# Performance work log

Hardware: AMD Instinct MI355X
Metric: run time of the kernel (lower is better)

Reference implementation:

```python
import jax, jax.numpy as jnp
import numpy as np

HIDDEN = 16  # hk.LSTM(16)


def lstm_scan(x, W, b, reverse):
    """Haiku LSTM unroll. x: [B,T,D]; W: [D+H, 4H]; b: [4H]. Returns [B,T,H]."""
    B = x.shape[0]

    def step(carry, xt):
        h, c = carry
        gated = jnp.concatenate([xt, h], axis=-1) @ W + b
        i, g, f, o = jnp.split(gated, 4, axis=-1)
        f = jax.nn.sigmoid(f + 1.0)  # haiku forget-gate bias of +1
        c = f * c + jax.nn.sigmoid(i) * jnp.tanh(g)
        h = jax.nn.sigmoid(o) * jnp.tanh(c)
        return (h, c), h

    init = (jnp.zeros((B, HIDDEN), x.dtype), jnp.zeros((B, HIDDEN), x.dtype))
    xt = jnp.swapaxes(x, 0, 1)  # [T,B,D] time-major for scan
    _, outs = jax.lax.scan(step, init, xt, reverse=reverse)
    return jnp.swapaxes(outs, 0, 1)  # [B,T,H]


def setup_inputs() -> dict:
    key = jax.random.key(0)
    ks = jax.random.split(key, 8)
    B, T, D = 4096, 256, 20
    E, H, M, OUT = 64, HIDDEN, 16, 2

    def glorot(k, shape):
        fan_in = shape[0]
        return (jax.random.normal(k, shape, jnp.float32) / np.sqrt(fan_in)).astype(jnp.float32)

    return {
        "x": jax.random.normal(ks[0], (B, T, D), jnp.float32),
        "W0": glorot(ks[1], (D, E)), "b0": jnp.zeros((E,), jnp.float32),
        "Wf": glorot(ks[2], (E + H, 4 * H)), "bf": jnp.zeros((4 * H,), jnp.float32),
        "Wb": glorot(ks[3], (E + H, 4 * H)), "bb": jnp.zeros((4 * H,), jnp.float32),
        "W1": glorot(ks[4], (2 * H, E)), "b1": jnp.zeros((E,), jnp.float32),
        "W2": glorot(ks[5], (E, M)), "b2": jnp.zeros((M,), jnp.float32),
        "W3": glorot(ks[6], (M, OUT)), "b3": jnp.zeros((OUT,), jnp.float32),
    }


def reference(x, W0, b0, Wf, bf, Wb, bb, W1, b1, W2, b2, W3, b3):
    h = jax.nn.relu(x @ W0 + b0)                 # [B,T,64]
    fwd = lstm_scan(h, Wf, bf, reverse=False)    # [B,T,16]
    bwd = lstm_scan(h, Wb, bb, reverse=True)     # [B,T,16], output[t] uses future state
    outs = jnp.concatenate([fwd, bwd], axis=-1)[:, -1, :]  # take last time step, [B,32]
    outs = jax.nn.relu(outs @ W1 + b1)
    outs = jax.nn.relu(outs @ W2 + b2)
    return outs @ W3 + b3
```

## Files before the change

### kernel.cpp

```cpp
#include <hip/hip_runtime.h>


typedef __attribute__((ext_vector_type(8))) short short8;
typedef __attribute__((ext_vector_type(4))) float floatx4;

union F8 { uint32_t u[4]; short8 v; };
union H2 { uint32_t u; _Float16 h[2]; };

#define LDW  66
#define LDW2 68

#define LOG2E 1.44269504088896340736f

__device__ __forceinline__ float tanh_fast(float x) {
    float e = __expf(-2.f * x);
    return __fdividef(2.f, 1.f + e) - 1.f;
}

#define ROT(v, S) __int_as_float(__builtin_amdgcn_mov_dpp(__float_as_int(v), 0x120 | (S), 0xf, 0xf, false))

__device__ __forceinline__ void split_pack(const float* f, uint32_t* hi, uint32_t* lo) {
#pragma unroll
    for (int i = 0; i < 4; ++i) {
        uint32_t u0 = __float_as_uint(f[2 * i]), u1 = __float_as_uint(f[2 * i + 1]);
        hi[i] = __builtin_amdgcn_perm(u1, u0, 0x07060302u);
        float r0 = f[2 * i]     - __uint_as_float(u0 & 0xFFFF0000u);
        float r1 = f[2 * i + 1] - __uint_as_float(u1 & 0xFFFF0000u);
        lo[i] = __builtin_amdgcn_perm(__float_as_uint(r1), __float_as_uint(r0), 0x07060302u);
    }
}

__global__ __launch_bounds__(256, 2)
void gpre_gemm(const float* __restrict__ x,
               const float* __restrict__ W0, const float* __restrict__ b0,
               const float* __restrict__ Wf, const float* __restrict__ bf,
               uint32_t* __restrict__ gph)
{
    __shared__ __align__(16) float tA[4][16 * LDW2];
    __shared__ __align__(16) float tB[4][16 * LDW2];

    const int tid  = threadIdx.x;
    const int wv   = tid >> 6;
    const int j    = tid & 63;
    const int nl   = j & 15;
    const int quad = j >> 4;

    F8 B1h[4], B1l[4];
#pragma unroll
    for (int T = 0; T < 4; ++T) {
        float w[8];
#pragma unroll
        for (int e = 0; e < 8; ++e) {
            int k = quad * 8 + e;
            w[e] = (k < 20) ? W0[k * 64 + T * 16 + nl] : 0.f;
        }
        split_pack(w, B1h[T].u, B1l[T].u);
    }
    F8 B2h[4][2], B2l[4][2];
#pragma unroll
    for (int T = 0; T < 4; ++T)
#pragma unroll
        for (int KH = 0; KH < 2; ++KH) {
            float w[8];
#pragma unroll
            for (int e = 0; e < 8; ++e) {
                int k = KH * 32 + quad * 8 + e;
                w[e] = Wf[k * 64 + T * 16 + nl];
            }
            split_pack(w, B2h[T][KH].u, B2l[T][KH].u);
        }

    float b0v[4], bfv[4];
#pragma unroll
    for (int T = 0; T < 4; ++T) {
        b0v[T] = b0[T * 16 + nl];
        bfv[T] = bf[T * 16 + nl] + ((T == 2) ? 1.f : 0.f);
    }

    const size_t base = (size_t)(blockIdx.x * 4 + wv) * 256;

    float4 xp0, xp1;
    {
        const float* xr = x + (base + nl) * 20;
        if (quad < 2) {
            xp0 = *(const float4*)(xr + quad * 8);
            xp1 = *(const float4*)(xr + quad * 8 + 4);
        } else if (quad == 2) {
            xp0 = *(const float4*)(xr + 16);
            xp1 = (float4){0.f, 0.f, 0.f, 0.f};
        } else {
            xp0 = (float4){0.f, 0.f, 0.f, 0.f};
            xp1 = (float4){0.f, 0.f, 0.f, 0.f};
        }
    }

#pragma unroll 1
    for (int tile = 0; tile < 16; ++tile) {
        float xk[8] = {xp0.x, xp0.y, xp0.z, xp0.w, xp1.x, xp1.y, xp1.z, xp1.w};

        {
            int tn = (tile < 15) ? (tile + 1) : 15;
            const float* xr = x + (base + tn * 16 + nl) * 20;
            if (quad < 2) {
                xp0 = *(const float4*)(xr + quad * 8);
                xp1 = *(const float4*)(xr + quad * 8 + 4);
            } else if (quad == 2) {
                xp0 = *(const float4*)(xr + 16);
            }
        }

        F8 A1h, A1l;
        split_pack(xk, A1h.u, A1l.u);

        floatx4 acc1[4];
#pragma unroll
        for (int T = 0; T < 4; ++T) acc1[T] = (floatx4){b0v[T], b0v[T], b0v[T], b0v[T]};
#pragma unroll
        for (int T = 0; T < 4; ++T) {
            acc1[T] = __builtin_amdgcn_mfma_f32_16x16x32_bf16(A1h.v, B1h[T].v, acc1[T], 0, 0, 0);
            acc1[T] = __builtin_amdgcn_mfma_f32_16x16x32_bf16(A1l.v, B1h[T].v, acc1[T], 0, 0, 0);
            acc1[T] = __builtin_amdgcn_mfma_f32_16x16x32_bf16(A1h.v, B1l[T].v, acc1[T], 0, 0, 0);
        }

#pragma unroll
        for (int T = 0; T < 4; ++T)
#pragma unroll
            for (int reg = 0; reg < 4; ++reg)
                tA[wv][(quad * 4 + reg) * LDW2 + T * 16 + nl] = fmaxf(acc1[T][reg], 0.f);
        __builtin_amdgcn_wave_barrier();

        F8 A2h[2], A2l[2];
#pragma unroll
        for (int KH = 0; KH < 2; ++KH) {
            float xe[8];
#pragma unroll
            for (int e = 0; e < 8; ++e)
                xe[e] = tA[wv][nl * LDW2 + KH * 32 + quad * 8 + e];
            split_pack(xe, A2h[KH].u, A2l[KH].u);
        }

        floatx4 acc2[4];
#pragma unroll
        for (int T = 0; T < 4; ++T) acc2[T] = (floatx4){bfv[T], bfv[T], bfv[T], bfv[T]};
#pragma unroll
        for (int T = 0; T < 4; ++T)
#pragma unroll
            for (int KH = 0; KH < 2; ++KH) {
                acc2[T] = __builtin_amdgcn_mfma_f32_16x16x32_bf16(A2h[KH].v, B2h[T][KH].v, acc2[T], 0, 0, 0);
                acc2[T] = __builtin_amdgcn_mfma_f32_16x16x32_bf16(A2l[KH].v, B2h[T][KH].v, acc2[T], 0, 0, 0);
                acc2[T] = __builtin_amdgcn_mfma_f32_16x16x32_bf16(A2h[KH].v, B2l[T][KH].v, acc2[T], 0, 0, 0);
            }

#pragma unroll
        for (int T = 0; T < 4; ++T)
#pragma unroll
            for (int reg = 0; reg < 4; ++reg)
                tB[wv][(quad * 4 + reg) * LDW2 + T * 16 + nl] = acc2[T][reg];
        __builtin_amdgcn_wave_barrier();

        uint32_t* gp = gph + ((base >> 1) + tile * 8) * 64;
#pragma unroll
        for (int tp = 0; tp < 8; ++tp) {
            float a0 = tB[wv][(2 * tp) * LDW2 + j];
            float a1 = tB[wv][(2 * tp + 1) * LDW2 + j];
            H2 pk;
            pk.h[0] = (_Float16)a0;
            pk.h[1] = (_Float16)a1;
            gp[tp * 64 + j] = pk.u;
        }
        __builtin_amdgcn_wave_barrier();
    }
}

__global__ __launch_bounds__(256, 4)
void lstm_scan(const uint32_t* __restrict__ gph,
               const float* __restrict__ x,
               const float* __restrict__ W0, const float* __restrict__ b0,
               const float* __restrict__ Wf,
               const float* __restrict__ Wb, const float* __restrict__ bb,
               const float* __restrict__ W1, const float* __restrict__ b1,
               const float* __restrict__ W2, const float* __restrict__ b2,
               const float* __restrict__ W3, const float* __restrict__ b3,
               float* __restrict__ out)
{
    __shared__ __align__(16) float xh_sh[4][64];
    __shared__ __align__(16) float h_sh[4][48];

    const int wv   = threadIdx.x >> 6;
    const int j    = threadIdx.x & 63;
    const int b    = blockIdx.x * 4 + wv;
    const int nl   = j & 15;
    const int quad = j >> 4;

    int rot1 = __builtin_amdgcn_mov_dpp(j, 0x121, 0xf, 0xf, false);
    const bool plus = ((rot1 & 15) == ((nl + 1) & 15));

    float wfhp[16];
#pragma unroll
    for (int s = 0; s < 16; ++s) {
        const int srcq = plus ? ((nl + s) & 15) : ((nl + 16 - s) & 15);
        wfhp[s] = Wf[(64 + srcq) * 64 + j];
    }

    const float gmul  = (quad == 1) ? -2.f : -1.f;
    const float gmul2 = gmul * LOG2E;
    const float amul  = (quad == 1) ? 2.f : 1.f;
    const float aadd  = (quad == 1) ? -1.f : 0.f;

    const int adr_i = 4 * nl;
    const int adr_g = 4 * nl + 64;
    const int adr_f = 4 * nl + 128;
    const int adr_o = 4 * nl + 192;

    float c = 0.f, hh = 0.f;
    const uint32_t* gb = gph + (size_t)b * (128 * 64);

#define STEPG(G)                                                               \
    {                                                                          \
        float v0 = (G), v1, v2, v3;                                            \
        asm volatile(                                                          \
            "v_fmac_f32 %0, %4, %5\n\t"                                        \
            "s_nop 1\n\t"                                                      \
            "v_mul_f32_dpp %1, %4, %6 row_ror:1 row_mask:0xf bank_mask:0xf\n\t"  \
            "v_mul_f32_dpp %2, %4, %7 row_ror:2 row_mask:0xf bank_mask:0xf\n\t"  \
            "v_mul_f32_dpp %3, %4, %8 row_ror:3 row_mask:0xf bank_mask:0xf\n\t"  \
            "v_fmac_f32_dpp %0, %4, %9 row_ror:4 row_mask:0xf bank_mask:0xf\n\t" \
            "v_fmac_f32_dpp %1, %4, %10 row_ror:5 row_mask:0xf bank_mask:0xf\n\t" \
            "v_fmac_f32_dpp %2, %4, %11 row_ror:6 row_mask:0xf bank_mask:0xf\n\t" \
            "v_fmac_f32_dpp %3, %4, %12 row_ror:7 row_mask:0xf bank_mask:0xf\n\t" \
            "v_fmac_f32_dpp %0, %4, %13 row_ror:8 row_mask:0xf bank_mask:0xf\n\t" \
            "v_fmac_f32_dpp %1, %4, %14 row_ror:9 row_mask:0xf bank_mask:0xf\n\t" \
            "v_fmac_f32_dpp %2, %4, %15 row_ror:10 row_mask:0xf bank_mask:0xf\n\t" \
            "v_fmac_f32_dpp %3, %4, %16 row_ror:11 row_mask:0xf bank_mask:0xf\n\t" \
            "v_fmac_f32_dpp %0, %4, %17 row_ror:12 row_mask:0xf bank_mask:0xf\n\t" \
            "v_fmac_f32_dpp %1, %4, %18 row_ror:13 row_mask:0xf bank_mask:0xf\n\t" \
            "v_fmac_f32_dpp %2, %4, %19 row_ror:14 row_mask:0xf bank_mask:0xf\n\t" \
            "v_fmac_f32_dpp %3, %4, %20 row_ror:15 row_mask:0xf bank_mask:0xf"   \
            : "+&v"(v0), "=&v"(v1), "=&v"(v2), "=&v"(v3)                       \
            : "v"(hh),                                                         \
              "v"(wfhp[0]),  "v"(wfhp[1]),  "v"(wfhp[2]),  "v"(wfhp[3]),       \
              "v"(wfhp[4]),  "v"(wfhp[5]),  "v"(wfhp[6]),  "v"(wfhp[7]),       \
              "v"(wfhp[8]),  "v"(wfhp[9]),  "v"(wfhp[10]), "v"(wfhp[11]),      \
              "v"(wfhp[12]), "v"(wfhp[13]), "v"(wfhp[14]), "v"(wfhp[15]));     \
        float gated = (v0 + v1) + (v2 + v3);                                   \
        float e = __builtin_amdgcn_exp2f(gmul2 * gated);                       \
        float y = __builtin_amdgcn_rcpf(1.f + e);                              \
        float a = fmaf(y, amul, aadd);                                         \
        int ab = __float_as_int(a);                                            \
        float ai = __int_as_float(__builtin_amdgcn_ds_bpermute(adr_i, ab));    \
        float ag = __int_as_float(__builtin_amdgcn_ds_bpermute(adr_g, ab));    \
        float af = __int_as_float(__builtin_amdgcn_ds_bpermute(adr_f, ab));    \
        float ao = __int_as_float(__builtin_amdgcn_ds_bpermute(adr_o, ab));    \
        c = fmaf(af, c, ai * ag);                                              \
        float e2 = __builtin_amdgcn_exp2f(-2.f * LOG2E * c);                   \
        float th = fmaf(__builtin_amdgcn_rcpf(1.f + e2), 2.f, -1.f);           \
        hh = ao * th;                                                          \
    }

    uint32_t bufA[8], bufB[8];
#pragma unroll
    for (int i = 0; i < 8; ++i) bufA[i] = gb[i * 64 + j];
#pragma unroll
    for (int i = 0; i < 8; ++i) bufB[i] = gb[(8 + i) * 64 + j];

#pragma unroll 1
    for (int blk = 0; blk < 16; blk += 2) {
#pragma unroll
        for (int p = 0; p < 8; ++p) {
            H2 u; u.u = bufA[p];
            float g0 = (float)u.h[0];
            float g1 = (float)u.h[1];
            STEPG(g0)
            STEPG(g1)
        }
        {
            int nb = blk + 2; nb = (nb > 15) ? 15 : nb;
#pragma unroll
            for (int i = 0; i < 8; ++i) bufA[i] = gb[(nb * 8 + i) * 64 + j];
        }
#pragma unroll
        for (int p = 0; p < 8; ++p) {
            H2 u; u.u = bufB[p];
            float g0 = (float)u.h[0];
            float g1 = (float)u.h[1];
            STEPG(g0)
            STEPG(g1)
        }
        {
            int nb = blk + 3; nb = (nb > 15) ? 15 : nb;
#pragma unroll
            for (int i = 0; i < 8; ++i) bufB[i] = gb[(nb * 8 + i) * 64 + j];
        }
    }
#undef STEPG

    {
        const float* xr = x + (size_t)b * (256 * 20) + 255 * 20;
        float s = b0[j];
#pragma unroll
        for (int k = 0; k < 20; ++k) s = fmaf(xr[k], W0[k * 64 + j], s);
        xh_sh[wv][j] = fmaxf(s, 0.f);
        if (j < 16) h_sh[wv][j] = hh;
    }
    __builtin_amdgcn_wave_barrier();

    {
        float u0 = bb[j], u1 = 0.f, u2 = 0.f, u3 = 0.f;
        const float* xr = xh_sh[wv];
#pragma unroll
        for (int k4 = 0; k4 < 16; ++k4) {
            u0 = fmaf(xr[4 * k4 + 0], Wb[(4 * k4 + 0) * 64 + j], u0);
            u1 = fmaf(xr[4 * k4 + 1], Wb[(4 * k4 + 1) * 64 + j], u1);
            u2 = fmaf(xr[4 * k4 + 2], Wb[(4 * k4 + 2) * 64 + j], u2);
            u3 = fmaf(xr[4 * k4 + 3], Wb[(4 * k4 + 3) * 64 + j], u3);
        }
        float gated = (u0 + u1) + (u2 + u3);
        float e = __expf(gmul * gated);
        float y = __fdividef(1.f, 1.f + e);
        float a = fmaf(y, amul, aadd);
        float ai = __shfl(a, nl, 64);
        float ag = __shfl(a, nl + 16, 64);
        float ao = __shfl(a, nl + 48, 64);
        float cb = ai * ag;
        float hb = ao * tanh_fast(cb);
        __builtin_amdgcn_wave_barrier();
        if (j < 16) h_sh[wv][16 + j] = hb;
        __builtin_amdgcn_wave_barrier();
    }

    {
        float u0 = b1[j], u1 = 0.f, u2 = 0.f, u3 = 0.f;
        const float4* hs = (const float4*)h_sh[wv];
#pragma unroll
        for (int k4 = 0; k4 < 8; ++k4) {
            float4 v = hs[k4];
            u0 = fmaf(v.x, W1[(4 * k4 + 0) * 64 + j], u0);
            u1 = fmaf(v.y, W1[(4 * k4 + 1) * 64 + j], u1);
            u2 = fmaf(v.z, W1[(4 * k4 + 2) * 64 + j], u2);
            u3 = fmaf(v.w, W1[(4 * k4 + 3) * 64 + j], u3);
        }
        float l1 = fmaxf((u0 + u1) + (u2 + u3), 0.f);
        __builtin_amdgcn_wave_barrier();
        xh_sh[wv][j] = l1;
        __builtin_amdgcn_wave_barrier();

        if (j < 16) {
            float v0 = b2[j], v1 = 0.f, v2 = 0.f, v3 = 0.f;
            const float4* ls = (const float4*)xh_sh[wv];
#pragma unroll
            for (int k4 = 0; k4 < 16; ++k4) {
                float4 v = ls[k4];
                v0 = fmaf(v.x, W2[(4 * k4 + 0) * 16 + j], v0);
                v1 = fmaf(v.y, W2[(4 * k4 + 1) * 16 + j], v1);
                v2 = fmaf(v.z, W2[(4 * k4 + 2) * 16 + j], v2);
                v3 = fmaf(v.w, W2[(4 * k4 + 3) * 16 + j], v3);
            }
            h_sh[wv][32 + j] = fmaxf((v0 + v1) + (v2 + v3), 0.f);
        }
        __builtin_amdgcn_wave_barrier();

        if (j < 2) {
            float o = b3[j];
#pragma unroll
            for (int k = 0; k < 16; ++k)
                o = fmaf(h_sh[wv][32 + k], W3[k * 2 + j], o);
            out[b * 2 + j] = o;
        }
    }
}

__global__ __launch_bounds__(64, 2)
void bilstm_fused_r4(const float* __restrict__ x,
                     const float* __restrict__ W0, const float* __restrict__ b0,
                     const float* __restrict__ Wf, const float* __restrict__ bf,
                     const float* __restrict__ Wb, const float* __restrict__ bb,
                     const float* __restrict__ W1, const float* __restrict__ b1,
                     const float* __restrict__ W2, const float* __restrict__ b2,
                     const float* __restrict__ W3, const float* __restrict__ b3,
                     float* __restrict__ out)
{
    __shared__ __align__(16) float lds_xh[16 * LDW];
    __shared__ __align__(16) float lds_g [16 * LDW];
    __shared__ __align__(16) float h_sh[48];

    const int j    = threadIdx.x;
    const int b    = blockIdx.x;
    const int nl   = j & 15;
    const int quad = j >> 4;

    int rot1 = __builtin_amdgcn_mov_dpp(j, 0x121, 0xf, 0xf, false);
    const bool plus = ((rot1 & 15) == ((nl + 1) & 15));

    float wfhp[16];
#pragma unroll
    for (int s = 0; s < 16; ++s) {
        const int srcq = plus ? ((nl + s) & 15) : ((nl + 16 - s) & 15);
        wfhp[s] = Wf[(64 + srcq) * 64 + j];
    }

    F8 B1h[4], B1l[4];
#pragma unroll
    for (int T = 0; T < 4; ++T) {
        float w[8];
#pragma unroll
        for (int e = 0; e < 8; ++e) {
            int k = quad * 8 + e;
            w[e] = (k < 20) ? W0[k * 64 + T * 16 + nl] : 0.f;
        }
        split_pack(w, B1h[T].u, B1l[T].u);
    }
    F8 B2h[4][2], B2l[4][2];
#pragma unroll
    for (int T = 0; T < 4; ++T)
#pragma unroll
        for (int KH = 0; KH < 2; ++KH) {
            float w[8];
#pragma unroll
            for (int e = 0; e < 8; ++e) {
                int k = KH * 32 + quad * 8 + e;
                w[e] = Wf[k * 64 + T * 16 + nl];
            }
            split_pack(w, B2h[T][KH].u, B2l[T][KH].u);
        }

    float b0v[4], bfv[4];
#pragma unroll
    for (int T = 0; T < 4; ++T) {
        b0v[T] = b0[T * 16 + nl];
        bfv[T] = bf[T * 16 + nl];
    }

    const float gmul  = (quad == 1) ? -2.f : -1.f;
    const float gbias = (quad == 2) ? 1.f : 0.f;
    const float amul  = (quad == 1) ? 2.f : 1.f;
    const float aadd  = (quad == 1) ? -1.f : 0.f;
    const bool  b0sel = (quad & 1) != 0;
    const bool  b1sel = (quad & 2) != 0;

    float c = 0.f, hh = 0.f;
    const float* xb = x + (size_t)b * (256 * 20);

#pragma unroll 1
    for (int ch = 0; ch < 16; ++ch) {
        const int t0 = ch * 16;
        const float* xrow = xb + (size_t)(t0 + nl) * 20;
        float xk[8];
#pragma unroll
        for (int e = 0; e < 8; ++e) {
            int k = quad * 8 + e;
            xk[e] = (k < 20) ? xrow[k] : 0.f;
        }
        F8 A1h, A1l;
        split_pack(xk, A1h.u, A1l.u);

        floatx4 acc1[4];
#pragma unroll
        for (int T = 0; T < 4; ++T) acc1[T] = (floatx4){b0v[T], b0v[T], b0v[T], b0v[T]};
#pragma unroll
        for (int T = 0; T < 4; ++T) {
            acc1[T] = __builtin_amdgcn_mfma_f32_16x16x32_bf16(A1h.v, B1h[T].v, acc1[T], 0, 0, 0);
            acc1[T] = __builtin_amdgcn_mfma_f32_16x16x32_bf16(A1l.v, B1h[T].v, acc1[T], 0, 0, 0);
            acc1[T] = __builtin_amdgcn_mfma_f32_16x16x32_bf16(A1h.v, B1l[T].v, acc1[T], 0, 0, 0);
        }
#pragma unroll
        for (int T = 0; T < 4; ++T)
#pragma unroll
            for (int reg = 0; reg < 4; ++reg)
                lds_xh[(quad * 4 + reg) * LDW + T * 16 + nl] = fmaxf(acc1[T][reg], 0.f);
        __builtin_amdgcn_wave_barrier();

        F8 A2h[2], A2l[2];
#pragma unroll
        for (int KH = 0; KH < 2; ++KH) {
            float xe[8];
#pragma unroll
            for (int e = 0; e < 8; ++e)
                xe[e] = lds_xh[nl * LDW + KH * 32 + quad * 8 + e];
            split_pack(xe, A2h[KH].u, A2l[KH].u);
        }

        floatx4 acc2[4];
#pragma unroll
        for (int T = 0; T < 4; ++T) acc2[T] = (floatx4){bfv[T], bfv[T], bfv[T], bfv[T]};
#pragma unroll
        for (int T = 0; T < 4; ++T)
#pragma unroll
            for (int KH = 0; KH < 2; ++KH) {
                acc2[T] = __builtin_amdgcn_mfma_f32_16x16x32_bf16(A2h[KH].v, B2h[T][KH].v, acc2[T], 0, 0, 0);
                acc2[T] = __builtin_amdgcn_mfma_f32_16x16x32_bf16(A2l[KH].v, B2h[T][KH].v, acc2[T], 0, 0, 0);
                acc2[T] = __builtin_amdgcn_mfma_f32_16x16x32_bf16(A2h[KH].v, B2l[T][KH].v, acc2[T], 0, 0, 0);
            }
#pragma unroll
        for (int T = 0; T < 4; ++T)
#pragma unroll
            for (int reg = 0; reg < 4; ++reg)
                lds_g[(quad * 4 + reg) * LDW + T * 16 + nl] = acc2[T][reg];
        __builtin_amdgcn_wave_barrier();

        float gcur = lds_g[j];
#pragma unroll
        for (int tau = 0; tau < 16; ++tau) {
            float gnext = lds_g[((tau < 15) ? (tau + 1) : 15) * LDW + j];
            float v0 = hh * wfhp[0];
            float v1 = ROT(hh, 1) * wfhp[1];
            float v2 = ROT(hh, 2) * wfhp[2];
            float v3 = ROT(hh, 3) * wfhp[3];
            v0 = fmaf(ROT(hh, 4),  wfhp[4],  v0);
            v1 = fmaf(ROT(hh, 5),  wfhp[5],  v1);
            v2 = fmaf(ROT(hh, 6),  wfhp[6],  v2);
            v3 = fmaf(ROT(hh, 7),  wfhp[7],  v3);
            v0 = fmaf(ROT(hh, 8),  wfhp[8],  v0);
            v1 = fmaf(ROT(hh, 9),  wfhp[9],  v1);
            v2 = fmaf(ROT(hh, 10), wfhp[10], v2);
            v3 = fmaf(ROT(hh, 11), wfhp[11], v3);
            v0 = fmaf(ROT(hh, 12), wfhp[12], v0);
            v1 = fmaf(ROT(hh, 13), wfhp[13], v1);
            v2 = fmaf(ROT(hh, 14), wfhp[14], v2);
            v3 = fmaf(ROT(hh, 15), wfhp[15], v3);
            float gated = gcur + ((v0 + v1) + (v2 + v3));

            float e = __expf(gmul * (gated + gbias));
            float y = __fdividef(1.f, 1.f + e);
            float a = fmaf(y, amul, aadd);

            float d1 = __shfl_xor(a, 16);
            float d2 = __shfl_xor(a, 32);
            float d3 = __shfl_xor(a, 48);
            float lo  = b0sel ? d1 : a;
            float hi  = b0sel ? d3 : d2;
            float lo1 = b0sel ? a  : d1;
            float hi1 = b0sel ? d2 : d3;
            float ai = b1sel ? hi  : lo;
            float ag = b1sel ? hi1 : lo1;
            float af = b1sel ? lo  : hi;
            float ao = b1sel ? lo1 : hi1;

            c  = fmaf(af, c, ai * ag);
            hh = ao * tanh_fast(c);
            gcur = gnext;
        }
    }

    if (j < 16) h_sh[j] = hh;
    __builtin_amdgcn_wave_barrier();

    {
        float u0 = bb[j], u1 = 0.f, u2 = 0.f, u3 = 0.f;
        const float* xr = &lds_xh[15 * LDW];
#pragma unroll
        for (int k4 = 0; k4 < 16; ++k4) {
            u0 = fmaf(xr[4 * k4 + 0], Wb[(4 * k4 + 0) * 64 + j], u0);
            u1 = fmaf(xr[4 * k4 + 1], Wb[(4 * k4 + 1) * 64 + j], u1);
            u2 = fmaf(xr[4 * k4 + 2], Wb[(4 * k4 + 2) * 64 + j], u2);
            u3 = fmaf(xr[4 * k4 + 3], Wb[(4 * k4 + 3) * 64 + j], u3);
        }
        float gated = (u0 + u1) + (u2 + u3);
        float e = __expf(gmul * gated);
        float y = __fdividef(1.f, 1.f + e);
        float a = fmaf(y, amul, aadd);
        float ai = __shfl(a, nl, 64);
        float ag = __shfl(a, nl + 16, 64);
        float ao = __shfl(a, nl + 48, 64);
        float cb = ai * ag;
        float hb = ao * tanh_fast(cb);
        __builtin_amdgcn_wave_barrier();
        if (j < 16) h_sh[16 + j] = hb;
        __builtin_amdgcn_wave_barrier();
    }

    {
        float u0 = b1[j], u1 = 0.f, u2 = 0.f, u3 = 0.f;
        const float4* hs = (const float4*)h_sh;
#pragma unroll
        for (int k4 = 0; k4 < 8; ++k4) {
            float4 v = hs[k4];
            u0 = fmaf(v.x, W1[(4 * k4 + 0) * 64 + j], u0);
            u1 = fmaf(v.y, W1[(4 * k4 + 1) * 64 + j], u1);
            u2 = fmaf(v.z, W1[(4 * k4 + 2) * 64 + j], u2);
            u3 = fmaf(v.w, W1[(4 * k4 + 3) * 64 + j], u3);
        }
        float l1 = fmaxf((u0 + u1) + (u2 + u3), 0.f);
        __builtin_amdgcn_wave_barrier();
        lds_g[j] = l1;
        __builtin_amdgcn_wave_barrier();

        if (j < 16) {
            float v0 = b2[j], v1 = 0.f, v2 = 0.f, v3 = 0.f;
            const float4* ls = (const float4*)lds_g;
#pragma unroll
            for (int k4 = 0; k4 < 16; ++k4) {
                float4 v = ls[k4];
                v0 = fmaf(v.x, W2[(4 * k4 + 0) * 16 + j], v0);
                v1 = fmaf(v.y, W2[(4 * k4 + 1) * 16 + j], v1);
                v2 = fmaf(v.z, W2[(4 * k4 + 2) * 16 + j], v2);
                v3 = fmaf(v.w, W2[(4 * k4 + 3) * 16 + j], v3);
            }
            h_sh[32 + j] = fmaxf((v0 + v1) + (v2 + v3), 0.f);
        }
        __builtin_amdgcn_wave_barrier();

        if (j < 2) {
            float o = b3[j];
#pragma unroll
            for (int k = 0; k < 16; ++k)
                o = fmaf(h_sh[32 + k], W3[k * 2 + j], o);
            out[b * 2 + j] = o;
        }
    }
}

extern "C" void kernel_launch(void* const* d_in, const int* in_sizes, int n_in,
                              void* d_out, int out_size, void* d_ws, size_t ws_size,
                              hipStream_t stream) {
    const float* x  = (const float*)d_in[0];
    const float* W0 = (const float*)d_in[1];
    const float* b0 = (const float*)d_in[2];
    const float* Wf = (const float*)d_in[3];
    const float* bf = (const float*)d_in[4];
    const float* Wb = (const float*)d_in[5];
    const float* bb = (const float*)d_in[6];
    const float* W1 = (const float*)d_in[7];
    const float* b1 = (const float*)d_in[8];
    const float* W2 = (const float*)d_in[9];
    const float* b2 = (const float*)d_in[10];
    const float* W3 = (const float*)d_in[11];
    const float* b3 = (const float*)d_in[12];
    float* outp = (float*)d_out;

    const size_t need = (size_t)4096 * 128 * 64 * sizeof(uint32_t);
    if (ws_size >= need) {
        uint32_t* gph = (uint32_t*)d_ws;
        hipLaunchKernelGGL(gpre_gemm, dim3(1024), dim3(256), 0, stream,
                           x, W0, b0, Wf, bf, gph);
        hipLaunchKernelGGL(lstm_scan, dim3(1024), dim3(256), 0, stream,
                           gph, x, W0, b0, Wf, Wb, bb, W1, b1, W2, b2, W3, b3, outp);
    } else {
        hipLaunchKernelGGL(bilstm_fused_r4, dim3(4096), dim3(64), 0, stream,
                           x, W0, b0, Wf, bf, Wb, bb, W1, b1, W2, b2, W3, b3, outp);
    }
}
```

Baseline: 261.9 us.

## Fold activation scales into LSTM weights and vectorize gate-precompute layout

The sigmoid/tanh exponent scale factors (-log2e, -2log2e) are folded into the precomputed input-projection weights, biases and recurrent weights, so each step drops a multiply. The cell state is kept in a pre-scaled domain by adjusting the g-gate affine, so tanh(c) needs no scale multiply either. The recurrent dot product now uses two accumulators instead of four, which removes adds but lengthens the dependency chain. The fp16 gate buffer layout becomes per-lane contiguous so writes and prefetches use 128-bit vector loads and stores instead of eight scalar accesses.

New measurement: 255.6 us, median of 4. 1.02x faster.

```diff
diff --git a/kernel.cpp b/kernel.cpp
--- a/kernel.cpp
+++ b/kernel.cpp
@@ -6,6 +6,7 @@
 
 union F8 { uint32_t u[4]; short8 v; };
 union H2 { uint32_t u; _Float16 h[2]; };
+union B8 { uint4 q[2]; uint32_t d[8]; };
 
 #define LDW  66
 #define LDW2 68
@@ -58,23 +59,26 @@
     }
     F8 B2h[4][2], B2l[4][2];
 #pragma unroll
-    for (int T = 0; T < 4; ++T)
+    for (int T = 0; T < 4; ++T) {
+        const float sgT = (T == 1) ? (-2.f * LOG2E) : (-LOG2E);
 #pragma unroll
         for (int KH = 0; KH < 2; ++KH) {
             float w[8];
 #pragma unroll
             for (int e = 0; e < 8; ++e) {
                 int k = KH * 32 + quad * 8 + e;
-                w[e] = Wf[k * 64 + T * 16 + nl];
+                w[e] = Wf[k * 64 + T * 16 + nl] * sgT;
             }
             split_pack(w, B2h[T][KH].u, B2l[T][KH].u);
         }
+    }
 
     float b0v[4], bfv[4];
 #pragma unroll
     for (int T = 0; T < 4; ++T) {
+        const float sgT = (T == 1) ? (-2.f * LOG2E) : (-LOG2E);
         b0v[T] = b0[T * 16 + nl];
-        bfv[T] = bf[T * 16 + nl] + ((T == 2) ? 1.f : 0.f);
+        bfv[T] = (bf[T * 16 + nl] + ((T == 2) ? 1.f : 0.f)) * sgT;
     }
 
     const size_t base = (size_t)(blockIdx.x * 4 + wv) * 256;
@@ -158,15 +162,20 @@
                 tB[wv][(quad * 4 + reg) * LDW2 + T * 16 + nl] = acc2[T][reg];
         __builtin_amdgcn_wave_barrier();
 
-        uint32_t* gp = gph + ((base >> 1) + tile * 8) * 64;
-#pragma unroll
-        for (int tp = 0; tp < 8; ++tp) {
-            float a0 = tB[wv][(2 * tp) * LDW2 + j];
-            float a1 = tB[wv][(2 * tp + 1) * LDW2 + j];
-            H2 pk;
-            pk.h[0] = (_Float16)a0;
-            pk.h[1] = (_Float16)a1;
-            gp[tp * 64 + j] = pk.u;
+        {
+            B8 r;
+#pragma unroll
+            for (int tp = 0; tp < 8; ++tp) {
+                float a0 = tB[wv][(2 * tp) * LDW2 + j];
+                float a1 = tB[wv][(2 * tp + 1) * LDW2 + j];
+                H2 pk;
+                pk.h[0] = (_Float16)a0;
+                pk.h[1] = (_Float16)a1;
+                r.d[tp] = pk.u;
+            }
+            uint32_t* gp = gph + ((size_t)(blockIdx.x * 4 + wv) * 16 + tile) * 512 + j * 8;
+            *(uint4*)(gp)     = r.q[0];
+            *(uint4*)(gp + 4) = r.q[1];
         }
         __builtin_amdgcn_wave_barrier();
     }
@@ -195,55 +204,57 @@
     int rot1 = __builtin_amdgcn_mov_dpp(j, 0x121, 0xf, 0xf, false);
     const bool plus = ((rot1 & 15) == ((nl + 1) & 15));
 
+    const float sj = (quad == 1) ? (-2.f * LOG2E) : (-LOG2E);
     float wfhp[16];
 #pragma unroll
     for (int s = 0; s < 16; ++s) {
         const int srcq = plus ? ((nl + s) & 15) : ((nl + 16 - s) & 15);
-        wfhp[s] = Wf[(64 + srcq) * 64 + j];
-    }
-
-    const float gmul  = (quad == 1) ? -2.f : -1.f;
-    const float gmul2 = gmul * LOG2E;
-    const float amul  = (quad == 1) ? 2.f : 1.f;
-    const float aadd  = (quad == 1) ? -1.f : 0.f;
+        wfhp[s] = Wf[(64 + srcq) * 64 + j] * sj;
+    }
+
+    const float amul = (quad == 1) ? (-4.f * LOG2E) : 1.f;
+    const float aadd = (quad == 1) ? ( 2.f * LOG2E) : 0.f;
+
+    const float gmulE = (quad == 1) ? -2.f : -1.f;
+    const float amulE = (quad == 1) ? 2.f : 1.f;
+    const float aaddE = (quad == 1) ? -1.f : 0.f;
 
     const int adr_i = 4 * nl;
     const int adr_g = 4 * nl + 64;
     const int adr_f = 4 * nl + 128;
     const int adr_o = 4 * nl + 192;
 
-    float c = 0.f, hh = 0.f;
-    const uint32_t* gb = gph + (size_t)b * (128 * 64);
+    float C = 0.f, hh = 0.f;
+    const uint32_t* gb = gph + (size_t)b * 8192;
 
 #define STEPG(G)                                                               \
     {                                                                          \
-        float v0 = (G), v1, v2, v3;                                            \
+        float v0 = (G), v1;                                                    \
         asm volatile(                                                          \
-            "v_fmac_f32 %0, %4, %5\n\t"                                        \
+            "v_fmac_f32 %0, %2, %3\n\t"                                        \
             "s_nop 1\n\t"                                                      \
-            "v_mul_f32_dpp %1, %4, %6 row_ror:1 row_mask:0xf bank_mask:0xf\n\t"  \
-            "v_mul_f32_dpp %2, %4, %7 row_ror:2 row_mask:0xf bank_mask:0xf\n\t"  \
-            "v_mul_f32_dpp %3, %4, %8 row_ror:3 row_mask:0xf bank_mask:0xf\n\t"  \
-            "v_fmac_f32_dpp %0, %4, %9 row_ror:4 row_mask:0xf bank_mask:0xf\n\t" \
-            "v_fmac_f32_dpp %1, %4, %10 row_ror:5 row_mask:0xf bank_mask:0xf\n\t" \
-            "v_fmac_f32_dpp %2, %4, %11 row_ror:6 row_mask:0xf bank_mask:0xf\n\t" \
-            "v_fmac_f32_dpp %3, %4, %12 row_ror:7 row_mask:0xf bank_mask:0xf\n\t" \
-            "v_fmac_f32_dpp %0, %4, %13 row_ror:8 row_mask:0xf bank_mask:0xf\n\t" \
-            "v_fmac_f32_dpp %1, %4, %14 row_ror:9 row_mask:0xf bank_mask:0xf\n\t" \
-            "v_fmac_f32_dpp %2, %4, %15 row_ror:10 row_mask:0xf bank_mask:0xf\n\t" \
-            "v_fmac_f32_dpp %3, %4, %16 row_ror:11 row_mask:0xf bank_mask:0xf\n\t" \
-            "v_fmac_f32_dpp %0, %4, %17 row_ror:12 row_mask:0xf bank_mask:0xf\n\t" \
-            "v_fmac_f32_dpp %1, %4, %18 row_ror:13 row_mask:0xf bank_mask:0xf\n\t" \
-            "v_fmac_f32_dpp %2, %4, %19 row_ror:14 row_mask:0xf bank_mask:0xf\n\t" \
-            "v_fmac_f32_dpp %3, %4, %20 row_ror:15 row_mask:0xf bank_mask:0xf"   \
-            : "+&v"(v0), "=&v"(v1), "=&v"(v2), "=&v"(v3)                       \
+            "v_mul_f32_dpp %1, %2, %4 row_ror:1 row_mask:0xf bank_mask:0xf\n\t"  \
+            "v_fmac_f32_dpp %0, %2, %5 row_ror:2 row_mask:0xf bank_mask:0xf\n\t" \
+            "v_fmac_f32_dpp %1, %2, %6 row_ror:3 row_mask:0xf bank_mask:0xf\n\t" \
+            "v_fmac_f32_dpp %0, %2, %7 row_ror:4 row_mask:0xf bank_mask:0xf\n\t" \
+            "v_fmac_f32_dpp %1, %2, %8 row_ror:5 row_mask:0xf bank_mask:0xf\n\t" \
+            "v_fmac_f32_dpp %0, %2, %9 row_ror:6 row_mask:0xf bank_mask:0xf\n\t" \
+            "v_fmac_f32_dpp %1, %2, %10 row_ror:7 row_mask:0xf bank_mask:0xf\n\t" \
+            "v_fmac_f32_dpp %0, %2, %11 row_ror:8 row_mask:0xf bank_mask:0xf\n\t" \
+            "v_fmac_f32_dpp %1, %2, %12 row_ror:9 row_mask:0xf bank_mask:0xf\n\t" \
+            "v_fmac_f32_dpp %0, %2, %13 row_ror:10 row_mask:0xf bank_mask:0xf\n\t" \
+            "v_fmac_f32_dpp %1, %2, %14 row_ror:11 row_mask:0xf bank_mask:0xf\n\t" \
+            "v_fmac_f32_dpp %0, %2, %15 row_ror:12 row_mask:0xf bank_mask:0xf\n\t" \
+            "v_fmac_f32_dpp %1, %2, %16 row_ror:13 row_mask:0xf bank_mask:0xf\n\t" \
+            "v_fmac_f32_dpp %0, %2, %17 row_ror:14 row_mask:0xf bank_mask:0xf\n\t" \
+            "v_fmac_f32_dpp %1, %2, %18 row_ror:15 row_mask:0xf bank_mask:0xf"   \
+            : "+&v"(v0), "=&v"(v1)                                             \
             : "v"(hh),                                                         \
               "v"(wfhp[0]),  "v"(wfhp[1]),  "v"(wfhp[2]),  "v"(wfhp[3]),       \
               "v"(wfhp[4]),  "v"(wfhp[5]),  "v"(wfhp[6]),  "v"(wfhp[7]),       \
               "v"(wfhp[8]),  "v"(wfhp[9]),  "v"(wfhp[10]), "v"(wfhp[11]),      \
               "v"(wfhp[12]), "v"(wfhp[13]), "v"(wfhp[14]), "v"(wfhp[15]));     \
-        float gated = (v0 + v1) + (v2 + v3);                                   \
-        float e = __builtin_amdgcn_exp2f(gmul2 * gated);                       \
+        float e = __builtin_amdgcn_exp2f(v0 + v1);                             \
         float y = __builtin_amdgcn_rcpf(1.f + e);                              \
         float a = fmaf(y, amul, aadd);                                         \
         int ab = __float_as_int(a);                                            \
@@ -251,23 +262,23 @@
         float ag = __int_as_float(__builtin_amdgcn_ds_bpermute(adr_g, ab));    \
         float af = __int_as_float(__builtin_amdgcn_ds_bpermute(adr_f, ab));    \
         float ao = __int_as_float(__builtin_amdgcn_ds_bpermute(adr_o, ab));    \
-        c = fmaf(af, c, ai * ag);                                              \
-        float e2 = __builtin_amdgcn_exp2f(-2.f * LOG2E * c);                   \
+        C = fmaf(af, C, ai * ag);                                              \
+        float e2 = __builtin_amdgcn_exp2f(C);                                  \
         float th = fmaf(__builtin_amdgcn_rcpf(1.f + e2), 2.f, -1.f);           \
         hh = ao * th;                                                          \
     }
 
-    uint32_t bufA[8], bufB[8];
-#pragma unroll
-    for (int i = 0; i < 8; ++i) bufA[i] = gb[i * 64 + j];
-#pragma unroll
-    for (int i = 0; i < 8; ++i) bufB[i] = gb[(8 + i) * 64 + j];
+    B8 bufA, bufB;
+    bufA.q[0] = *(const uint4*)(gb + j * 8);
+    bufA.q[1] = *(const uint4*)(gb + j * 8 + 4);
+    bufB.q[0] = *(const uint4*)(gb + 512 + j * 8);
+    bufB.q[1] = *(const uint4*)(gb + 512 + j * 8 + 4);
 
 #pragma unroll 1
     for (int blk = 0; blk < 16; blk += 2) {
 #pragma unroll
         for (int p = 0; p < 8; ++p) {
-            H2 u; u.u = bufA[p];
+            H2 u; u.u = bufA.d[p];
             float g0 = (float)u.h[0];
             float g1 = (float)u.h[1];
             STEPG(g0)
@@ -275,12 +286,12 @@
         }
         {
             int nb = blk + 2; nb = (nb > 15) ? 15 : nb;
-#pragma unroll
-            for (int i = 0; i < 8; ++i) bufA[i] = gb[(nb * 8 + i) * 64 + j];
+            bufA.q[0] = *(const uint4*)(gb + nb * 512 + j * 8);
+            bufA.q[1] = *(const uint4*)(gb + nb * 512 + j * 8 + 4);
         }
 #pragma unroll
         for (int p = 0; p < 8; ++p) {
-            H2 u; u.u = bufB[p];
+            H2 u; u.u = bufB.d[p];
             float g0 = (float)u.h[0];
             float g1 = (float)u.h[1];
             STEPG(g0)
@@ -288,8 +299,8 @@
         }
         {
             int nb = blk + 3; nb = (nb > 15) ? 15 : nb;
-#pragma unroll
-            for (int i = 0; i < 8; ++i) bufB[i] = gb[(nb * 8 + i) * 64 + j];
+            bufB.q[0] = *(const uint4*)(gb + nb * 512 + j * 8);
+            bufB.q[1] = *(const uint4*)(gb + nb * 512 + j * 8 + 4);
         }
     }
 #undef STEPG
@@ -315,9 +326,9 @@
             u3 = fmaf(xr[4 * k4 + 3], Wb[(4 * k4 + 3) * 64 + j], u3);
         }
         float gated = (u0 + u1) + (u2 + u3);
-        float e = __expf(gmul * gated);
+        float e = __expf(gmulE * gated);
         float y = __fdividef(1.f, 1.f + e);
-        float a = fmaf(y, amul, aadd);
+        float a = fmaf(y, amulE, aaddE);
         float ai = __shfl(a, nl, 64);
         float ag = __shfl(a, nl + 16, 64);
         float ao = __shfl(a, nl + 48, 64);
```
